# Kernel tuning notes

Hardware: AMD Instinct MI355X
Metric: run time of the kernel (lower is better)

The kernel has to match this reference:

```python
import jax, jax.numpy as jnp
import numpy as np

DIM = 128
NUM_LAYERS = 2
FF_MULT = 4
RADIUS = 0.2
K = 8
B, N, L = 8, 2048, 4096
NEG = -1e30


def setup_inputs() -> dict:
    key = jax.random.key(0)
    ks = jax.random.split(key, 12)
    C = DIM
    s = 1.0 / np.sqrt(C)
    w = lambda k, shape, sc: jax.random.normal(k, shape, dtype=jnp.float32) * sc
    inp = {
        "q_xyz": jax.random.uniform(ks[0], (B, N, 3), dtype=jnp.float32),
        "q_feat": jax.random.normal(ks[1], (B, N, C), dtype=jnp.float32),
        "kv_xyz": jax.random.uniform(ks[2], (B, L, 3), dtype=jnp.float32),
        "kv_feat": jax.random.normal(ks[3], (B, L, C), dtype=jnp.float32),
        "kv_pad": jnp.zeros((B, L), dtype=bool),
        # PointTransformerConv params (stacked over layers)
        "W_lin": w(ks[4], (NUM_LAYERS, C, C), s),   # value projection (with bias)
        "b_lin": jnp.zeros((NUM_LAYERS, C), jnp.float32),
        "W_src": w(ks[5], (NUM_LAYERS, C, C), s),   # lin_src, no bias
        "W_dst": w(ks[6], (NUM_LAYERS, C, C), s),   # lin_dst, no bias
        "W_attn": w(ks[7], (NUM_LAYERS, C, C), s),  # attn_nn = Linear+ReLU
        "b_attn": jnp.zeros((NUM_LAYERS, C), jnp.float32),
        "ln1_g": jnp.ones((NUM_LAYERS, C), jnp.float32),
        "ln1_b": jnp.zeros((NUM_LAYERS, C), jnp.float32),
        "W_ff1": w(ks[8], (NUM_LAYERS, C, FF_MULT * C), s),
        "b_ff1": jnp.zeros((NUM_LAYERS, FF_MULT * C), jnp.float32),
        "W_ff2": w(ks[9], (NUM_LAYERS, FF_MULT * C, C), 1.0 / np.sqrt(FF_MULT * C)),
        "b_ff2": jnp.zeros((NUM_LAYERS, C), jnp.float32),
        "ln2_g": jnp.ones((NUM_LAYERS, C), jnp.float32),
        "ln2_b": jnp.zeros((NUM_LAYERS, C), jnp.float32),
    }
    return inp


def _layernorm(x, g, b):
    mu = x.mean(-1, keepdims=True)
    var = ((x - mu) ** 2).mean(-1, keepdims=True)
    return (x - mu) * jax.lax.rsqrt(var + 1e-5) * g + b


def _gather(feats, idx):
    # feats: [B, L, C], idx: [B, N, K] -> [B, N, K, C]
    b, n, k = idx.shape
    g = jnp.take_along_axis(feats, idx.reshape(b, n * k)[:, :, None], axis=1)
    return g.reshape(b, n, k, feats.shape[-1])


def _forward(q_xyz, q_feat, kv_xyz, kv_feat, kv_pad,
             W_lin, b_lin, W_src, W_dst, W_attn, b_attn,
             ln1_g, ln1_b, W_ff1, b_ff1, W_ff2, b_ff2, ln2_g, ln2_b):
    # radius neighbor search (per-batch, fixed K neighbors with validity mask)
    d2 = jnp.sum((q_xyz[:, :, None, :] - kv_xyz[:, None, :, :]) ** 2, axis=-1)  # [B,N,L]
    valid_pair = (d2 <= RADIUS * RADIUS) & (~kv_pad)[:, None, :]
    negd = jnp.where(valid_pair, -d2, NEG)
    negv, idx = jax.lax.top_k(negd, K)          # [B,N,K] nearest-in-ball
    evalid = negv > 0.5 * NEG                   # edge validity mask [B,N,K]

    out = q_feat
    for i in range(NUM_LAYERS):
        # PointTransformerConv, pos_nn = ZeroPos => delta = 0
        aj = _gather(kv_feat @ W_src[i], idx)                    # [B,N,K,C]
        vj = _gather(kv_feat @ W_lin[i] + b_lin[i], idx)         # [B,N,K,C]
        ai = out @ W_dst[i]                                      # [B,N,C]
        logits = jax.nn.relu((ai[:, :, None, :] - aj) @ W_attn[i] + b_attn[i])
        logits = jnp.where(evalid[..., None], logits, NEG)
        m = logits.max(axis=2, keepdims=True)
        e = jnp.exp(logits - m) * evalid[..., None]
        attn = e / jnp.maximum(e.sum(axis=2, keepdims=True), 1e-9)  # per-channel softmax over neighbors
        upd = jnp.sum(attn * vj, axis=2)                         # [B,N,C] scatter-add over edges
        out = _layernorm(out + upd, ln1_g[i], ln1_b[i])
        h = jax.nn.gelu(out @ W_ff1[i] + b_ff1[i], approximate=False)
        out = _layernorm(out + h @ W_ff2[i] + b_ff2[i], ln2_g[i], ln2_b[i])
    return out


def reference(q_xyz, q_feat, kv_xyz, kv_feat, kv_pad,
              W_lin, b_lin, W_src, W_dst, W_attn, b_attn,
              ln1_g, ln1_b, W_ff1, b_ff1, W_ff2, b_ff2, ln2_g, ln2_b):
    return _forward(q_xyz, q_feat, kv_xyz, kv_feat, kv_pad,
                    W_lin, b_lin, W_src, W_dst, W_attn, b_attn,
                    ln1_g, ln1_b, W_ff1, b_ff1, W_ff2, b_ff2, ln2_g, ln2_b)
```

## Files before the change

kernel.cpp:

```cpp
#include <hip/hip_runtime.h>
#include <hip/hip_bf16.h>
#include <math.h>

#define DIM 128
#define BB 8
#define NN 2048
#define LL 4096
#define KK 8

typedef __hip_bfloat16 bf16;
typedef __attribute__((ext_vector_type(8))) short short8;
typedef __attribute__((ext_vector_type(4))) float float4v;

__device__ __forceinline__ float toF(float x){ return x; }
__device__ __forceinline__ float toF(bf16 x){ return __bfloat162float(x); }
__device__ __forceinline__ void st(float* p, float v){ *p = v; }
__device__ __forceinline__ void st(bf16*  p, float v){ *p = __float2bfloat16(v); }
__device__ __forceinline__ unsigned short f2bf(float f){
  union { bf16 b; unsigned short u; } cv; cv.b = __float2bfloat16(f); return cv.u;
}

__device__ __forceinline__ float gelu_exact(float x){
  return 0.5f * x * (1.0f + erff(x * 0.70710678118654752f));
}

__device__ __forceinline__ float waveSum64(float v){
  #pragma unroll
  for (int o = 32; o > 0; o >>= 1) v += __shfl_xor(v, o, 64);
  return v;
}
__device__ __forceinline__ float quadSum16(float v){
  #pragma unroll
  for (int o = 8; o > 0; o >>= 1) v += __shfl_xor(v, o, 64);
  return v;
}

__device__ __forceinline__ void topk_insert(float (&bd)[KK], int (&bi)[KK], float d2, int id){
  bd[KK-1] = d2; bi[KK-1] = id;
  #pragma unroll
  for (int s = KK-1; s > 0; --s){
    if (bd[s] < bd[s-1]){
      float td = bd[s]; bd[s] = bd[s-1]; bd[s-1] = td;
      int   ti = bi[s]; bi[s] = bi[s-1]; bi[s-1] = ti;
    }
  }
}

#define KCHUNK 1024
#define QBLK 8
#define SPL 32
__global__ __launch_bounds__(256) void knn_kernel(const float* __restrict__ q_xyz,
                                                  const float* __restrict__ kv_xyz,
                                                  int* __restrict__ idx)
{
  __shared__ float4 kp[KCHUNK];
  const int tid  = threadIdx.x;
  const int s    = tid >> 3;
  const int qloc = tid & 7;
  const int b    = blockIdx.y;
  const int qbase = blockIdx.x * QBLK;
  const size_t qo = ((size_t)b * NN + qbase + qloc) * 3;
  const float qx = q_xyz[qo], qy = q_xyz[qo+1], qz = q_xyz[qo+2];
  const float THR0 = __uint_as_float(0x3D23D70Bu);
  float thr = THR0;
  float bd[KK]; int bi[KK];
  #pragma unroll
  for (int k = 0; k < KK; k++){ bd[k] = 3e38f; bi[k] = -1; }
  const float* kvp = kv_xyz + (size_t)b * LL * 3;
  for (int c0 = 0; c0 < LL; c0 += KCHUNK){
    __syncthreads();
    {
      const float4* src = (const float4*)(kvp + (size_t)c0 * 3);
      const float4 a  = src[3*tid];
      const float4 b4 = src[3*tid + 1];
      const float4 c4 = src[3*tid + 2];
      kp[4*tid + 0] = make_float4(a.x,  a.y,  a.z,  0.f);
      kp[4*tid + 1] = make_float4(a.w,  b4.x, b4.y, 0.f);
      kp[4*tid + 2] = make_float4(b4.z, b4.w, c4.x, 0.f);
      kp[4*tid + 3] = make_float4(c4.y, c4.z, c4.w, 0.f);
    }
    __syncthreads();
    #pragma unroll 8
    for (int j = 0; j < KCHUNK/SPL; j++){
      const int e = (j << 5) + s;
      const float4 pnt = kp[e];
      const float dx = qx - pnt.x, dy = qy - pnt.y, dz = qz - pnt.z;
      const float d2 = dx*dx + dy*dy + dz*dz;
      if (d2 < thr){
        topk_insert(bd, bi, d2, c0 + e);
        thr = fminf(bd[KK-1], THR0);
      }
    }
  }
  __syncthreads();
  float* cd = (float*)kp;
  int*   ci = (int*)((char*)kp + 8192);
  #pragma unroll
  for (int k = 0; k < KK; k++){
    const int row = s*KK + k;
    cd[row*QBLK + qloc] = bd[k];
    ci[row*QBLK + qloc] = bi[k];
  }
  __syncthreads();
  if (tid < QBLK){
    float md[KK]; int mi[KK];
    #pragma unroll
    for (int k = 0; k < KK; k++){ md[k] = 3e38f; mi[k] = -1; }
    for (int j = 0; j < SPL*KK; j++){
      const float d = cd[j*QBLK + tid];
      if (d < md[KK-1]) topk_insert(md, mi, d, ci[j*QBLK + tid]);
    }
    const int q = b * NN + qbase + tid;
    #pragma unroll
    for (int k = 0; k < KK; k++) idx[q*KK + k] = mi[k];
  }
}

__device__ __forceinline__ void packOne(const float* __restrict__ src,
                                        bf16* __restrict__ dst, int idx, int nshift){
  const int k = idx >> nshift;
  const int n = idx & ((1 << nshift) - 1);
  const int N = 1 << nshift;
  st(&dst[((size_t)(k>>3)*N + n)*8 + (k&7)], src[idx]);
}

__global__ void packW_all(const float* __restrict__ Wlin, const float* __restrict__ Wff1,
                          const float* __restrict__ Wff2, bf16* __restrict__ WlinP,
                          bf16* __restrict__ Wff1P, bf16* __restrict__ Wff2P){
  int i = blockIdx.x*256 + threadIdx.x;
  if (i < 32768){
    const int l = i >> 14, r = i & 16383;
    packOne(Wlin + (size_t)l*16384, WlinP + (size_t)l*16384, r, 7);
  } else if (i < 163840){
    i -= 32768;
    const int l = i >> 16, r = i & 65535;
    packOne(Wff1 + (size_t)l*65536, Wff1P + (size_t)l*65536, r, 9);
  } else if (i < 294912){
    i -= 163840;
    const int l = i >> 16, r = i & 65535;
    packOne(Wff2 + (size_t)l*65536, Wff2P + (size_t)l*65536, r, 7);
  }
}

__global__ __launch_bounds__(128) void wcomb_pack(const float* __restrict__ Wsrc,
                                                  const float* __restrict__ Wdst,
                                                  const float* __restrict__ Wattn,
                                                  bf16* __restrict__ WsaP,
                                                  bf16* __restrict__ WdaP)
{
  __shared__ float row[DIM];
  const int r = blockIdx.x, c = threadIdx.x, which = blockIdx.y, lay = blockIdx.z;
  const float* Wx = (which ? Wdst : Wsrc) + (size_t)lay*DIM*DIM;
  const float* Wa = Wattn + (size_t)lay*DIM*DIM;
  row[c] = Wx[r*DIM + c];
  __syncthreads();
  float acc = 0.f;
  for (int j = 0; j < DIM; j++) acc = fmaf(row[j], Wa[j*DIM + c], acc);
  bf16* dst = (which ? WdaP : WsaP) + (size_t)lay*DIM*DIM;
  st(&dst[((size_t)(r>>3)*DIM + c)*8 + (r&7)], acc);
}

__device__ __forceinline__ void stage_A_f32(const float* __restrict__ A, size_t r0,
                                            int kd, int kc, unsigned short* As, int tid){
  #pragma unroll
  for (int i = 0; i < 8; i++){
    const int f = tid + i*256;
    const int row = f >> 5, c4 = (f & 31) * 4;
    const float4 v = *(const float4*)&A[(r0+row)*kd + kc + c4];
    uint2 u;
    u.x = (unsigned)f2bf(v.x) | ((unsigned)f2bf(v.y) << 16);
    u.y = (unsigned)f2bf(v.z) | ((unsigned)f2bf(v.w) << 16);
    *(uint2*)&As[row*136 + c4] = u;
  }
}
__device__ __forceinline__ void stage_A_bf16(const bf16* __restrict__ A, size_t r0,
                                             int kd, int kc, unsigned short* As, int tid){
  #pragma unroll
  for (int i = 0; i < 8; i++){
    const int f = tid + i*256;
    const int row = f >> 5, c4 = (f & 31) * 4;
    *(uint2*)&As[row*136 + c4] = *(const uint2*)&A[(r0+row)*kd + kc + c4];
  }
}

template<typename TA, int NDIM, bool GELU>
__global__ __launch_bounds__(256) void mfma_single(const TA* __restrict__ A,
                                                   const bf16* __restrict__ Wp,
                                                   const float* __restrict__ bias,
                                                   bf16* __restrict__ Y)
{
  __shared__ __align__(16) unsigned short As[64*136];
  const int tid = threadIdx.x;
  const size_t r0 = (size_t)blockIdx.x * 64;
  const int nblk = blockIdx.y * 128;
  if (sizeof(TA) == 4) stage_A_f32((const float*)A, r0, 128, 0, As, tid);
  else                 stage_A_bf16((const bf16*)A, r0, 128, 0, As, tid);
  __syncthreads();
  const int wid = tid >> 6, ln = tid & 63, qd = ln >> 4, cl = ln & 15;
  float4v acc[8];
  #pragma unroll
  for (int t = 0; t < 8; t++) acc[t] = (float4v){0.f,0.f,0.f,0.f};
  #pragma unroll
  for (int ks = 0; ks < 4; ks++){
    const short8 a = *(const short8*)&As[(wid*16 + cl)*136 + (ks*4 + qd)*8];
    const short8* wb = (const short8*)Wp + (size_t)(ks*4 + qd)*NDIM + nblk + cl;
    #pragma unroll
    for (int t = 0; t < 8; t++){
      const short8 b = wb[t*16];
      acc[t] = __builtin_amdgcn_mfma_f32_16x16x32_bf16(a, b, acc[t], 0, 0, 0);
    }
  }
  #pragma unroll
  for (int t = 0; t < 8; t++){
    const int col = nblk + t*16 + cl;
    const float bv = bias ? bias[col] : 0.f;
    #pragma unroll
    for (int r = 0; r < 4; r++){
      const size_t row = r0 + wid*16 + qd*4 + r;
      float v = acc[t][r] + bv;
      if (GELU) v = gelu_exact(v);
      st(&Y[row*NDIM + col], v);
    }
  }
}

__global__ __launch_bounds__(256) void mfma_dual(const float* __restrict__ A,
                                                 const bf16* __restrict__ Wp0,
                                                 const bf16* __restrict__ Wp1,
                                                 const float* __restrict__ bias1,
                                                 bf16* __restrict__ Y0,
                                                 bf16* __restrict__ Y1)
{
  __shared__ __align__(16) unsigned short As[64*136];
  const int tid = threadIdx.x;
  const size_t r0 = (size_t)blockIdx.x * 64;
  stage_A_f32(A, r0, 128, 0, As, tid);
  __syncthreads();
  const int wid = tid >> 6, ln = tid & 63, qd = ln >> 4, cl = ln & 15;
  float4v ac0[8], ac1[8];
  #pragma unroll
  for (int t = 0; t < 8; t++){ ac0[t] = (float4v){0.f,0.f,0.f,0.f}; ac1[t] = (float4v){0.f,0.f,0.f,0.f}; }
  #pragma unroll
  for (int ks = 0; ks < 4; ks++){
    const short8 a = *(const short8*)&As[(wid*16 + cl)*136 + (ks*4 + qd)*8];
    const size_t wo = (size_t)(ks*4 + qd)*DIM + cl;
    const short8* wb0 = (const short8*)Wp0 + wo;
    const short8* wb1 = (const short8*)Wp1 + wo;
    #pragma unroll
    for (int t = 0; t < 8; t++){
      const short8 b0 = wb0[t*16];
      ac0[t] = __builtin_amdgcn_mfma_f32_16x16x32_bf16(a, b0, ac0[t], 0, 0, 0);
      const short8 b1 = wb1[t*16];
      ac1[t] = __builtin_amdgcn_mfma_f32_16x16x32_bf16(a, b1, ac1[t], 0, 0, 0);
    }
  }
  #pragma unroll
  for (int t = 0; t < 8; t++){
    const int col = t*16 + cl;
    const float bv = bias1[col];
    #pragma unroll
    for (int r = 0; r < 4; r++){
      const size_t row = r0 + wid*16 + qd*4 + r;
      st(&Y0[row*DIM + col], ac0[t][r]);
      st(&Y1[row*DIM + col], ac1[t][r] + bv);
    }
  }
}

__global__ __launch_bounds__(256) void mfma_ff2ln(const bf16* __restrict__ A,
                                                  const bf16* __restrict__ Wp,
                                                  const float* __restrict__ b2,
                                                  const bf16* __restrict__ resid,
                                                  const float* __restrict__ g,
                                                  const float* __restrict__ bb,
                                                  float* __restrict__ Y)
{
  __shared__ __align__(16) unsigned short As[64*136];
  const int tid = threadIdx.x;
  const size_t r0 = (size_t)blockIdx.x * 64;
  const int wid = tid >> 6, ln = tid & 63, qd = ln >> 4, cl = ln & 15;
  float4v acc[8];
  #pragma unroll
  for (int t = 0; t < 8; t++) acc[t] = (float4v){0.f,0.f,0.f,0.f};
  for (int kc = 0; kc < 512; kc += 128){
    __syncthreads();
    stage_A_bf16(A, r0, 512, kc, As, tid);
    __syncthreads();
    const int k8c = kc >> 3;
    #pragma unroll
    for (int ks = 0; ks < 4; ks++){
      const short8 a = *(const short8*)&As[(wid*16 + cl)*136 + (ks*4 + qd)*8];
      const short8* wb = (const short8*)Wp + (size_t)(k8c + ks*4 + qd)*DIM + cl;
      #pragma unroll
      for (int t = 0; t < 8; t++){
        const short8 b = wb[t*16];
        acc[t] = __builtin_amdgcn_mfma_f32_16x16x32_bf16(a, b, acc[t], 0, 0, 0);
      }
    }
  }
  float v[8][4];
  #pragma unroll
  for (int t = 0; t < 8; t++){
    const int col = t*16 + cl;
    const float bv = b2[col];
    #pragma unroll
    for (int r = 0; r < 4; r++){
      const size_t row = r0 + wid*16 + qd*4 + r;
      v[t][r] = acc[t][r] + bv + toF(resid[row*DIM + col]);
    }
  }
  #pragma unroll
  for (int r = 0; r < 4; r++){
    float s = 0.f;
    #pragma unroll
    for (int t = 0; t < 8; t++) s += v[t][r];
    const float mu = quadSum16(s) * (1.f/DIM);
    float q = 0.f;
    #pragma unroll
    for (int t = 0; t < 8; t++){ const float d = v[t][r] - mu; q += d*d; }
    const float inv = rsqrtf(quadSum16(q) * (1.f/DIM) + 1e-5f);
    const size_t row = r0 + wid*16 + qd*4 + r;
    #pragma unroll
    for (int t = 0; t < 8; t++){
      const int col = t*16 + cl;
      Y[row*DIM + col] = (v[t][r] - mu) * inv * g[col] + bb[col];
    }
  }
}

__global__ __launch_bounds__(256) void attn_ln1(const bf16* __restrict__ qA,
                                                const bf16* __restrict__ srcA,
                                                const bf16* __restrict__ linp,
                                                const int* __restrict__ idx,
                                                const float* __restrict__ b_attn,
                                                const float* __restrict__ feat,
                                                const float* __restrict__ g,
                                                const float* __restrict__ bb,
                                                bf16* __restrict__ out1)
{
  const int tid = threadIdx.x;
  const int wv = tid >> 6, ln = tid & 63;
  const int q = blockIdx.x * 4 + wv;
  const int b = q >> 11;
  const bf16* sbase = srcA + (size_t)b * LL * DIM;
  const bf16* vbase = linp + (size_t)b * LL * DIM;
  const int c0 = ln, c1 = ln + 64;
  const float qa0 = toF(qA[(size_t)q*DIM + c0]) + b_attn[c0];
  const float qa1 = toF(qA[(size_t)q*DIM + c1]) + b_attn[c1];
  int ids[KK]; float l0[KK], l1[KK];
  float m0 = -1e30f, m1 = -1e30f;
  #pragma unroll
  for (int k = 0; k < KK; k++){
    const int id = idx[q*KK + k]; ids[k] = id;
    if (id >= 0){
      const float s0 = toF(sbase[(size_t)id*DIM + c0]);
      const float s1 = toF(sbase[(size_t)id*DIM + c1]);
      l0[k] = fmaxf(qa0 - s0, 0.f); m0 = fmaxf(m0, l0[k]);
      l1[k] = fmaxf(qa1 - s1, 0.f); m1 = fmaxf(m1, l1[k]);
    } else { l0[k] = 0.f; l1[k] = 0.f; }
  }
  float sum0 = 0.f, sum1 = 0.f, upd0 = 0.f, upd1 = 0.f;
  #pragma unroll
  for (int k = 0; k < KK; k++) if (ids[k] >= 0){
    const float e0 = expf(l0[k] - m0); l0[k] = e0; sum0 += e0;
    const float e1 = expf(l1[k] - m1); l1[k] = e1; sum1 += e1;
  }
  if (sum0 > 0.f){
    const float i0 = 1.f / sum0, i1 = 1.f / sum1;
    #pragma unroll
    for (int k = 0; k < KK; k++) if (ids[k] >= 0){
      upd0 = fmaf(l0[k]*i0, toF(vbase[(size_t)ids[k]*DIM + c0]), upd0);
      upd1 = fmaf(l1[k]*i1, toF(vbase[(size_t)ids[k]*DIM + c1]), upd1);
    }
  }
  const float x0 = feat[(size_t)q*DIM + c0] + upd0;
  const float x1 = feat[(size_t)q*DIM + c1] + upd1;
  const float mu = waveSum64(x0 + x1) * (1.f/DIM);
  const float d0 = x0 - mu, d1 = x1 - mu;
  const float var = waveSum64(d0*d0 + d1*d1) * (1.f/DIM);
  const float inv = rsqrtf(var + 1e-5f);
  st(&out1[(size_t)q*DIM + c0], d0 * inv * g[c0] + bb[c0]);
  st(&out1[(size_t)q*DIM + c1], d1 * inv * g[c1] + bb[c1]);
}

extern "C" void kernel_launch(void* const* d_in, const int* in_sizes, int n_in,
                              void* d_out, int out_size, void* d_ws, size_t ws_size,
                              hipStream_t stream)
{
  const float* q_xyz  = (const float*)d_in[0];
  const float* q_feat = (const float*)d_in[1];
  const float* kv_xyz = (const float*)d_in[2];
  const float* kv_feat= (const float*)d_in[3];
  const float* W_lin  = (const float*)d_in[5];
  const float* b_lin  = (const float*)d_in[6];
  const float* W_src  = (const float*)d_in[7];
  const float* W_dst  = (const float*)d_in[8];
  const float* W_attn = (const float*)d_in[9];
  const float* b_attn = (const float*)d_in[10];
  const float* ln1_g  = (const float*)d_in[11];
  const float* ln1_b  = (const float*)d_in[12];
  const float* W_ff1  = (const float*)d_in[13];
  const float* b_ff1  = (const float*)d_in[14];
  const float* W_ff2  = (const float*)d_in[15];
  const float* b_ff2  = (const float*)d_in[16];
  const float* ln2_g  = (const float*)d_in[17];
  const float* ln2_b  = (const float*)d_in[18];
  float* out = (float*)d_out;

  const int MQ  = BB * NN;
  const int MKV = BB * LL;

  char* p = (char*)d_ws;
  int*   idxb  = (int*)p;   p += (size_t)MQ * KK * 4;
  bf16*  WsaP  = (bf16*)p;  p += (size_t)2 * DIM * DIM * 2;
  bf16*  WdaP  = (bf16*)p;  p += (size_t)2 * DIM * DIM * 2;
  bf16*  WlinP = (bf16*)p;  p += (size_t)2 * DIM * DIM * 2;
  bf16*  Wff1P = (bf16*)p;  p += (size_t)2 * DIM * 4*DIM * 2;
  bf16*  Wff2P = (bf16*)p;  p += (size_t)2 * 4*DIM * DIM * 2;
  float* feat  = (float*)p; p += (size_t)MQ * DIM * 4;
  bf16*  out1  = (bf16*)p;  p += (size_t)MQ * DIM * 2;
  bf16*  srcA  = (bf16*)p;  p += (size_t)MKV * DIM * 2;
  bf16*  linp  = (bf16*)p;  p += (size_t)MKV * DIM * 2;
  bf16*  qA    = (bf16*)p;  p += (size_t)MQ * DIM * 2;
  bf16*  hbuf  = srcA;

  knn_kernel<<<dim3(NN/QBLK, BB), 256, 0, stream>>>(q_xyz, kv_xyz, idxb);
  packW_all<<<(294912 + 255)/256, 256, 0, stream>>>(W_lin, W_ff1, W_ff2,
                                                    WlinP, Wff1P, Wff2P);
  wcomb_pack<<<dim3(DIM, 2, 2), DIM, 0, stream>>>(W_src, W_dst, W_attn, WsaP, WdaP);

  for (int i = 0; i < 2; i++){
    const size_t w128 = (size_t)i * DIM * DIM;
    const size_t w512 = (size_t)i * DIM * 4*DIM;
    const float* featIn = (i == 0) ? q_feat : feat;

    mfma_dual<<<MKV/64, 256, 0, stream>>>(kv_feat, WsaP + w128, WlinP + w128,
                                          b_lin + i*DIM, srcA, linp);
    mfma_single<float, 128, false><<<MQ/64, 256, 0, stream>>>(featIn, WdaP + w128,
                                                              nullptr, qA);
    attn_ln1<<<MQ/4, 256, 0, stream>>>(qA, srcA, linp, idxb, b_attn + i*DIM, featIn,
                                       ln1_g + i*DIM, ln1_b + i*DIM, out1);
    mfma_single<bf16, 512, true><<<dim3(MQ/64, 4), 256, 0, stream>>>(
        out1, Wff1P + w512, b_ff1 + i*4*DIM, hbuf);
    float* ydst = (i == 1) ? out : feat;
    mfma_ff2ln<<<MQ/64, 256, 0, stream>>>(hbuf, Wff2P + w512, b_ff2 + i*DIM, out1,
                                          ln2_g + i*DIM, ln2_b + i*DIM, ydst);
  }
}
```

Before: 354.1 us.

## Merge weight-prep and projection launches; parallelize KNN candidate merge

Fuses the two weight-packing kernels into one launch and merges the kv dual projection with the query projection into a single grid, cutting kernel launches and tail underutilization. The KNN final merge now runs in two stages: 64 threads each reduce 4 slices, then 8 threads merge 64 candidates each. Before, 8 threads scanned 256 candidates. The merge uses packed 64-bit distance/index keys for the comparisons and a padded shared layout to avoid bank conflicts. The kv staging loop is simplified to scalar loads, which may be slightly less efficient than the previous float4 loads.

```diff
diff --git a/kernel.cpp b/kernel.cpp
--- a/kernel.cpp
+++ b/kernel.cpp
@@ -9,6 +9,7 @@
 #define KK 8
 
 typedef __hip_bfloat16 bf16;
+typedef unsigned long long ull;
 typedef __attribute__((ext_vector_type(8))) short short8;
 typedef __attribute__((ext_vector_type(4))) float float4v;
 
@@ -45,6 +46,13 @@
     }
   }
 }
+__device__ __forceinline__ void topk_insert_u(ull (&m)[KK], ull key){
+  m[KK-1] = key;
+  #pragma unroll
+  for (int t = KK-1; t > 0; --t){
+    if (m[t] < m[t-1]){ ull tmp = m[t]; m[t] = m[t-1]; m[t-1] = tmp; }
+  }
+}
 
 #define KCHUNK 1024
 #define QBLK 8
@@ -53,7 +61,10 @@
                                                   const float* __restrict__ kv_xyz,
                                                   int* __restrict__ idx)
 {
-  __shared__ float4 kp[KCHUNK];
+  __shared__ __align__(16) float smem[4112];
+  float4* kp = (float4*)smem;
+  float*  cd = smem;
+  int*    ci = (int*)(smem + 2056);
   const int tid  = threadIdx.x;
   const int s    = tid >> 3;
   const int qloc = tid & 7;
@@ -69,15 +80,9 @@
   const float* kvp = kv_xyz + (size_t)b * LL * 3;
   for (int c0 = 0; c0 < LL; c0 += KCHUNK){
     __syncthreads();
-    {
-      const float4* src = (const float4*)(kvp + (size_t)c0 * 3);
-      const float4 a  = src[3*tid];
-      const float4 b4 = src[3*tid + 1];
-      const float4 c4 = src[3*tid + 2];
-      kp[4*tid + 0] = make_float4(a.x,  a.y,  a.z,  0.f);
-      kp[4*tid + 1] = make_float4(a.w,  b4.x, b4.y, 0.f);
-      kp[4*tid + 2] = make_float4(b4.z, b4.w, c4.x, 0.f);
-      kp[4*tid + 3] = make_float4(c4.y, c4.z, c4.w, 0.f);
+    for (int e = tid; e < KCHUNK; e += 256){
+      const size_t o = (size_t)(c0 + e) * 3;
+      kp[e] = make_float4(kvp[o], kvp[o+1], kvp[o+2], 0.f);
     }
     __syncthreads();
     #pragma unroll 8
@@ -93,26 +98,47 @@
     }
   }
   __syncthreads();
-  float* cd = (float*)kp;
-  int*   ci = (int*)((char*)kp + 8192);
   #pragma unroll
   for (int k = 0; k < KK; k++){
-    const int row = s*KK + k;
-    cd[row*QBLK + qloc] = bd[k];
-    ci[row*QBLK + qloc] = bi[k];
+    const int a = qloc*257 + s*8 + k;
+    cd[a] = bd[k];
+    ci[a] = bi[k];
   }
   __syncthreads();
-  if (tid < QBLK){
-    float md[KK]; int mi[KK];
-    #pragma unroll
-    for (int k = 0; k < KK; k++){ md[k] = 3e38f; mi[k] = -1; }
-    for (int j = 0; j < SPL*KK; j++){
-      const float d = cd[j*QBLK + tid];
-      if (d < md[KK-1]) topk_insert(md, mi, d, ci[j*QBLK + tid]);
-    }
-    const int q = b * NN + qbase + tid;
-    #pragma unroll
-    for (int k = 0; k < KK; k++) idx[q*KK + k] = mi[k];
+  if (tid < 64){
+    const int q = tid >> 3, g = tid & 7;
+    ull m[KK];
+    #pragma unroll
+    for (int k = 0; k < KK; k++) m[k] = ~0ULL;
+    #pragma unroll
+    for (int mm = 0; mm < 4; mm++){
+      const int sl = g + 8*mm;
+      #pragma unroll
+      for (int k = 0; k < KK; k++){
+        const int a = q*257 + sl*8 + k;
+        const ull key = ((ull)__float_as_uint(cd[a]) << 32) | (unsigned)ci[a];
+        if (key < m[KK-1]) topk_insert_u(m, key);
+      }
+    }
+    #pragma unroll
+    for (int k = 0; k < KK; k++){
+      const int a = q*257 + g*8 + k;
+      cd[a] = __uint_as_float((unsigned)(m[k] >> 32));
+      ci[a] = (int)(unsigned)(m[k] & 0xFFFFFFFFu);
+    }
+    if (tid < QBLK){
+      ull f[KK];
+      #pragma unroll
+      for (int k = 0; k < KK; k++) f[k] = ~0ULL;
+      for (int j = 0; j < 64; j++){
+        const int a = tid*257 + j;
+        const ull key = ((ull)__float_as_uint(cd[a]) << 32) | (unsigned)ci[a];
+        if (key < f[KK-1]) topk_insert_u(f, key);
+      }
+      const int q = b * NN + qbase + tid;
+      #pragma unroll
+      for (int k = 0; k < KK; k++) idx[q*KK + k] = (int)(unsigned)(f[k] & 0xFFFFFFFFu);
+    }
   }
 }
 
@@ -124,40 +150,48 @@
   st(&dst[((size_t)(k>>3)*N + n)*8 + (k&7)], src[idx]);
 }
 
-__global__ void packW_all(const float* __restrict__ Wlin, const float* __restrict__ Wff1,
-                          const float* __restrict__ Wff2, bf16* __restrict__ WlinP,
-                          bf16* __restrict__ Wff1P, bf16* __restrict__ Wff2P){
-  int i = blockIdx.x*256 + threadIdx.x;
-  if (i < 32768){
-    const int l = i >> 14, r = i & 16383;
-    packOne(Wlin + (size_t)l*16384, WlinP + (size_t)l*16384, r, 7);
-  } else if (i < 163840){
-    i -= 32768;
-    const int l = i >> 16, r = i & 65535;
-    packOne(Wff1 + (size_t)l*65536, Wff1P + (size_t)l*65536, r, 9);
-  } else if (i < 294912){
-    i -= 163840;
-    const int l = i >> 16, r = i & 65535;
-    packOne(Wff2 + (size_t)l*65536, Wff2P + (size_t)l*65536, r, 7);
-  }
-}
-
-__global__ __launch_bounds__(128) void wcomb_pack(const float* __restrict__ Wsrc,
-                                                  const float* __restrict__ Wdst,
-                                                  const float* __restrict__ Wattn,
-                                                  bf16* __restrict__ WsaP,
-                                                  bf16* __restrict__ WdaP)
-{
-  __shared__ float row[DIM];
-  const int r = blockIdx.x, c = threadIdx.x, which = blockIdx.y, lay = blockIdx.z;
-  const float* Wx = (which ? Wdst : Wsrc) + (size_t)lay*DIM*DIM;
-  const float* Wa = Wattn + (size_t)lay*DIM*DIM;
-  row[c] = Wx[r*DIM + c];
-  __syncthreads();
-  float acc = 0.f;
-  for (int j = 0; j < DIM; j++) acc = fmaf(row[j], Wa[j*DIM + c], acc);
-  bf16* dst = (which ? WdaP : WsaP) + (size_t)lay*DIM*DIM;
-  st(&dst[((size_t)(r>>3)*DIM + c)*8 + (r&7)], acc);
+__global__ __launch_bounds__(256) void prep_weights(const float* __restrict__ Wlin,
+                                                    const float* __restrict__ Wff1,
+                                                    const float* __restrict__ Wff2,
+                                                    const float* __restrict__ Wsrc,
+                                                    const float* __restrict__ Wdst,
+                                                    const float* __restrict__ Wattn,
+                                                    bf16* __restrict__ WlinP,
+                                                    bf16* __restrict__ Wff1P,
+                                                    bf16* __restrict__ Wff2P,
+                                                    bf16* __restrict__ WsaP,
+                                                    bf16* __restrict__ WdaP)
+{
+  __shared__ float row[2][DIM];
+  const int bid = blockIdx.x;
+  if (bid < 1152){
+    int i = bid*256 + threadIdx.x;
+    if (i < 32768){
+      const int l = i >> 14, r = i & 16383;
+      packOne(Wlin + (size_t)l*16384, WlinP + (size_t)l*16384, r, 7);
+    } else if (i < 163840){
+      i -= 32768;
+      const int l = i >> 16, r = i & 65535;
+      packOne(Wff1 + (size_t)l*65536, Wff1P + (size_t)l*65536, r, 9);
+    } else if (i < 294912){
+      i -= 163840;
+      const int l = i >> 16, r = i & 65535;
+      packOne(Wff2 + (size_t)l*65536, Wff2P + (size_t)l*65536, r, 7);
+    }
+  } else {
+    const int half = threadIdx.x >> 7;
+    const int c = threadIdx.x & 127;
+    const int tt = (bid - 1152)*2 + half;
+    const int r = tt & 127, which = (tt >> 7) & 1, lay = tt >> 8;
+    const float* Wx = (which ? Wdst : Wsrc) + (size_t)lay*DIM*DIM;
+    const float* Wa = Wattn + (size_t)lay*DIM*DIM;
+    row[half][c] = Wx[r*DIM + c];
+    __syncthreads();
+    float acc = 0.f;
+    for (int j = 0; j < DIM; j++) acc = fmaf(row[half][j], Wa[j*DIM + c], acc);
+    bf16* dst = (which ? WdaP : WsaP) + (size_t)lay*DIM*DIM;
+    st(&dst[((size_t)(r>>3)*DIM + c)*8 + (r&7)], acc);
+  }
 }
 
 __device__ __forceinline__ void stage_A_f32(const float* __restrict__ A, size_t r0,
@@ -224,45 +258,76 @@
   }
 }
 
-__global__ __launch_bounds__(256) void mfma_dual(const float* __restrict__ A,
-                                                 const bf16* __restrict__ Wp0,
-                                                 const bf16* __restrict__ Wp1,
-                                                 const float* __restrict__ bias1,
-                                                 bf16* __restrict__ Y0,
-                                                 bf16* __restrict__ Y1)
+__global__ __launch_bounds__(256) void mfma_dual_qa(const float* __restrict__ kvf,
+                                                    const float* __restrict__ featIn,
+                                                    const bf16* __restrict__ Wp0,
+                                                    const bf16* __restrict__ Wp1,
+                                                    const bf16* __restrict__ WpQ,
+                                                    const float* __restrict__ bias1,
+                                                    bf16* __restrict__ Y0,
+                                                    bf16* __restrict__ Y1,
+                                                    bf16* __restrict__ Yq)
 {
   __shared__ __align__(16) unsigned short As[64*136];
   const int tid = threadIdx.x;
-  const size_t r0 = (size_t)blockIdx.x * 64;
-  stage_A_f32(A, r0, 128, 0, As, tid);
-  __syncthreads();
   const int wid = tid >> 6, ln = tid & 63, qd = ln >> 4, cl = ln & 15;
-  float4v ac0[8], ac1[8];
-  #pragma unroll
-  for (int t = 0; t < 8; t++){ ac0[t] = (float4v){0.f,0.f,0.f,0.f}; ac1[t] = (float4v){0.f,0.f,0.f,0.f}; }
-  #pragma unroll
-  for (int ks = 0; ks < 4; ks++){
-    const short8 a = *(const short8*)&As[(wid*16 + cl)*136 + (ks*4 + qd)*8];
-    const size_t wo = (size_t)(ks*4 + qd)*DIM + cl;
-    const short8* wb0 = (const short8*)Wp0 + wo;
-    const short8* wb1 = (const short8*)Wp1 + wo;
+  if (blockIdx.x < 512){
+    const size_t r0 = (size_t)blockIdx.x * 64;
+    stage_A_f32(kvf, r0, 128, 0, As, tid);
+    __syncthreads();
+    float4v ac0[8], ac1[8];
+    #pragma unroll
+    for (int t = 0; t < 8; t++){ ac0[t] = (float4v){0.f,0.f,0.f,0.f}; ac1[t] = (float4v){0.f,0.f,0.f,0.f}; }
+    #pragma unroll
+    for (int ks = 0; ks < 4; ks++){
+      const short8 a = *(const short8*)&As[(wid*16 + cl)*136 + (ks*4 + qd)*8];
+      const size_t wo = (size_t)(ks*4 + qd)*DIM + cl;
+      const short8* wb0 = (const short8*)Wp0 + wo;
+      const short8* wb1 = (const short8*)Wp1 + wo;
+      #pragma unroll
+      for (int t = 0; t < 8; t++){
+        const short8 b0 = wb0[t*16];
+        ac0[t] = __builtin_amdgcn_mfma_f32_16x16x32_bf16(a, b0, ac0[t], 0, 0, 0);
+        const short8 b1 = wb1[t*16];
+        ac1[t] = __builtin_amdgcn_mfma_f32_16x16x32_bf16(a, b1, ac1[t], 0, 0, 0);
+      }
+    }
     #pragma unroll
     for (int t = 0; t < 8; t++){
-      const short8 b0 = wb0[t*16];
-      ac0[t] = __builtin_amdgcn_mfma_f32_16x16x32_bf16(a, b0, ac0[t], 0, 0, 0);
-      const short8 b1 = wb1[t*16];
-      ac1[t] = __builtin_amdgcn_mfma_f32_16x16x32_bf16(a, b1, ac1[t], 0, 0, 0);
-    }
-  }
-  #pragma unroll
-  for (int t = 0; t < 8; t++){
-    const int col = t*16 + cl;
-    const float bv = bias1[col];
-    #pragma unroll
-    for (int r = 0; r < 4; r++){
-      const size_t row = r0 + wid*16 + qd*4 + r;
-      st(&Y0[row*DIM + col], ac0[t][r]);
-      st(&Y1[row*DIM + col], ac1[t][r] + bv);
+      const int col = t*16 + cl;
+      const float bv = bias1[col];
+      #pragma unroll
+      for (int r = 0; r < 4; r++){
+        const size_t row = r0 + wid*16 + qd*4 + r;
+        st(&Y0[row*DIM + col], ac0[t][r]);
+        st(&Y1[row*DIM + col], ac1[t][r] + bv);
+      }
+    }
+  } else {
+    const size_t r0 = (size_t)(blockIdx.x - 512) * 64;
+    stage_A_f32(featIn, r0, 128, 0, As, tid);
+    __syncthreads();
+    float4v acc[8];
+    #pragma unroll
+    for (int t = 0; t < 8; t++) acc[t] = (float4v){0.f,0.f,0.f,0.f};
+    #pragma unroll
+    for (int ks = 0; ks < 4; ks++){
+      const short8 a = *(const short8*)&As[(wid*16 + cl)*136 + (ks*4 + qd)*8];
+      const short8* wb = (const short8*)WpQ + (size_t)(ks*4 + qd)*DIM + cl;
+      #pragma unroll
+      for (int t = 0; t < 8; t++){
+        const short8 b = wb[t*16];
+        acc[t] = __builtin_amdgcn_mfma_f32_16x16x32_bf16(a, b, acc[t], 0, 0, 0);
+      }
+    }
+    #pragma unroll
+    for (int t = 0; t < 8; t++){
+      const int col = t*16 + cl;
+      #pragma unroll
+      for (int r = 0; r < 4; r++){
+        const size_t row = r0 + wid*16 + qd*4 + r;
+        st(&Yq[row*DIM + col], acc[t][r]);
+      }
     }
   }
 }
@@ -425,19 +490,16 @@
   bf16*  hbuf  = srcA;
 
   knn_kernel<<<dim3(NN/QBLK, BB), 256, 0, stream>>>(q_xyz, kv_xyz, idxb);
-  packW_all<<<(294912 + 255)/256, 256, 0, stream>>>(W_lin, W_ff1, W_ff2,
-                                                    WlinP, Wff1P, Wff2P);
-  wcomb_pack<<<dim3(DIM, 2, 2), DIM, 0, stream>>>(W_src, W_dst, W_attn, WsaP, WdaP);
+  prep_weights<<<1152 + 256, 256, 0, stream>>>(W_lin, W_ff1, W_ff2, W_src, W_dst,
+                                               W_attn, WlinP, Wff1P, Wff2P, WsaP, WdaP);
 
   for (int i = 0; i < 2; i++){
     const size_t w128 = (size_t)i * DIM * DIM;
     const size_t w512 = (size_t)i * DIM * 4*DIM;
     const float* featIn = (i == 0) ? q_feat : feat;
 
-    mfma_dual<<<MKV/64, 256, 0, stream>>>(kv_feat, WsaP + w128, WlinP + w128,
-                                          b_lin + i*DIM, srcA, linp);
-    mfma_single<float, 128, false><<<MQ/64, 256, 0, stream>>>(featIn, WdaP + w128,
-                                                              nullptr, qA);
+    mfma_dual_qa<<<MKV/64 + MQ/64, 256, 0, stream>>>(kv_feat, featIn,
+        WsaP + w128, WlinP + w128, WdaP + w128, b_lin + i*DIM, srcA, linp, qA);
     attn_ln1<<<MQ/4, 256, 0, stream>>>(qA, srcA, linp, idxb, b_attn + i*DIM, featIn,
                                        ln1_g + i*DIM, ln1_b + i*DIM, out1);
     mfma_single<bf16, 512, true><<<dim3(MQ/64, 4), 256, 0, stream>>>(
```

Result: faster. 333.3 us (-5.9%).
